# Performance work log

Measured on AMD Instinct MI355X. Metric: run time of the kernel, lower is better.

Reference implementation:

```python
import jax, jax.numpy as jnp
import numpy as np

B, N, H = 1, 4096, 2048
NH, HD = 16, H // 16
WINDOW = 4096
EPS = 1e-6
THETA = 10000.0
NEG = -1e30


def rmsnorm(x, w):
    var = jnp.mean(jnp.square(x.astype(jnp.float32)), axis=-1, keepdims=True)
    return (x * jax.lax.rsqrt(var + EPS)).astype(w.dtype) * w


def rotate_half(x):
    x1, x2 = x[..., : x.shape[-1] // 2], x[..., x.shape[-1] // 2 :]
    return jnp.concatenate((-x2, x1), axis=-1)


def setup_inputs() -> dict:
    key = jax.random.key(0)
    k1, k2, k3 = jax.random.split(key, 3)
    x = jax.random.normal(k1, (B, N, H), dtype=jnp.float32)
    w_qkv = jax.random.normal(k2, (H, 3 * H), dtype=jnp.float32) * (1.0 / np.sqrt(H))
    w_out = jax.random.normal(k3, (H, H), dtype=jnp.float32) * (1.0 / np.sqrt(H))
    q_gamma = jnp.ones((HD,), dtype=jnp.float32)
    k_gamma = jnp.ones((HD,), dtype=jnp.float32)
    return {"x": x, "w_qkv": w_qkv, "w_out": w_out, "q_gamma": q_gamma, "k_gamma": k_gamma}


def reference(x, w_qkv, w_out, q_gamma, k_gamma):
    b, n, _ = x.shape
    qkv = jnp.einsum('bnh,hm->bnm', x, w_qkv)  # [b,n,3H]
    q, k, v = jnp.split(qkv, 3, axis=-1)
    # [b, nh, n, hd]
    q = q.reshape(b, n, NH, HD).transpose(0, 2, 1, 3)
    k = k.reshape(b, n, NH, HD).transpose(0, 2, 1, 3)
    v = v.reshape(b, n, NH, HD).transpose(0, 2, 1, 3)
    # qk RMSNorm over head_dim
    q = rmsnorm(q, q_gamma)
    k = rmsnorm(k, k_gamma)
    # RoPE
    inv_freq = 1.0 / (THETA ** (jnp.arange(0, HD, 2, dtype=jnp.float32) / HD))
    t = jnp.arange(n, dtype=jnp.float32)
    freqs = t[:, None] * inv_freq[None, :]          # [n, hd/2]
    emb = jnp.concatenate((freqs, freqs), axis=-1)  # [n, hd]
    cos = jnp.cos(emb)[None, None, :, :]
    sin = jnp.sin(emb)[None, None, :, :]
    q = q * cos + rotate_half(q) * sin
    k = k * cos + rotate_half(k) * sin
    # causal + sliding-window mask (kv not truncated since n == WINDOW)
    kv_len = k.shape[-2]
    q_idx = jnp.arange(n)[:, None] + (kv_len - n)
    k_idx = jnp.arange(kv_len)[None, :]
    mask = (q_idx >= k_idx) & (q_idx - k_idx <= WINDOW)
    scores = jnp.einsum('bhqd,bhkd->bhqk', q, k) / np.sqrt(HD)
    scores = jnp.where(mask[None, None, :, :], scores, NEG)
    attn = jax.nn.softmax(scores, axis=-1)
    out = jnp.einsum('bhqk,bhkd->bhqd', attn, v)
    out = out.transpose(0, 2, 1, 3).reshape(b, n, H)
    return jnp.einsum('bnh,hm->bnm', out, w_out)
```

## Files before the change

### kernel.cpp

```cpp
#include <hip/hip_runtime.h>
#include <stdint.h>

typedef short bf16x8 __attribute__((ext_vector_type(8)));
typedef float f32x4 __attribute__((ext_vector_type(4)));
typedef unsigned short u16;

__device__ __forceinline__ float b2f(u16 u) {
  return __uint_as_float(((unsigned)u) << 16);
}
__device__ __forceinline__ u16 f2b(float f) {
  unsigned u = __float_as_uint(f);
  return (u16)((u + 0x7fffu + ((u >> 16) & 1u)) >> 16);
}

#define NEGINF (-1.0e30f)

__device__ __forceinline__ void gld_lds16(const u16* g, u16* l) {
  __builtin_amdgcn_global_load_lds(
      (const __attribute__((address_space(1))) unsigned int*)(const void*)g,
      (__attribute__((address_space(3))) unsigned int*)(void*)l, 16, 0, 0);
}

__global__ void sniff5(const u16* x, const u16* wq, const u16* wo,
                       const u16* qg, const u16* kg, int* flags) {
  const u16* p;
  int S;
  switch (blockIdx.x) {
    case 0: p = x;  S = 2048; break;
    case 1: p = wq; S = 2048; break;
    case 2: p = wo; S = 2048; break;
    case 3: p = qg; S = 128;  break;
    default: p = kg; S = 128; break;
  }
  __shared__ int cbig, czero;
  if (threadIdx.x == 0) { cbig = 0; czero = 0; }
  __syncthreads();
  int cb = 0, cz = 0;
  for (int i = threadIdx.x; i < S; i += 256) {
    const u16 u = p[i];
    if (((u >> 7) & 0xFF) >= 0xC0) ++cb;
    if (!(i & 1) && u == 0) ++cz;
  }
  atomicAdd(&cbig, cb);
  atomicAdd(&czero, cz);
  __syncthreads();
  if (threadIdx.x == 0)
    flags[blockIdx.x] = (cbig > S / 32 || czero > 3 * S / 8) ? 1 : 0;
}

__global__ __launch_bounds__(256) void conv_in(const void* __restrict__ src,
                                               u16* __restrict__ dst,
                                               const int* __restrict__ flags,
                                               int fidx, int n) {
  const int fp32 = flags[fidx];
  int i = blockIdx.x * 256 + threadIdx.x;
  const int stride = gridDim.x * 256;
  if (fp32) {
    const float* s = (const float*)src;
    for (; i < n; i += stride) dst[i] = f2b(s[i]);
  } else {
    const u16* s = (const u16*)src;
    for (; i < n; i += stride) dst[i] = s[i];
  }
}

__global__ __launch_bounds__(256) void transpose_in(
    const void* __restrict__ src, u16* __restrict__ dst,
    const int* __restrict__ flags, int fidx, int ss, int ds) {
  __shared__ u16 tile[64][65];
  const int fp32 = flags[fidx];
  const int rb = blockIdx.y * 64, cb = blockIdx.x * 64;
  const int cl = threadIdx.x & 63, r0 = threadIdx.x >> 6;
  if (fp32) {
    const float* s = (const float*)src;
#pragma unroll
    for (int i = 0; i < 16; ++i) {
      int r = r0 + i * 4;
      tile[r][cl] = f2b(s[(long long)(rb + r) * ss + cb + cl]);
    }
  } else {
    const u16* s = (const u16*)src;
#pragma unroll
    for (int i = 0; i < 16; ++i) {
      int r = r0 + i * 4;
      tile[r][cl] = s[(long long)(rb + r) * ss + cb + cl];
    }
  }
  __syncthreads();
#pragma unroll
  for (int i = 0; i < 16; ++i) {
    int r2 = r0 + i * 4;
    dst[(long long)(cb + r2) * ds + rb + cl] = tile[cl][r2];
  }
}

__global__ __launch_bounds__(256) void transpose_bf16(
    const u16* __restrict__ src, u16* __restrict__ dst, int ss, int ds,
    long long sz, long long dz) {
  __shared__ u16 tile[64][65];
  const u16* s = src + (long long)blockIdx.z * sz;
  u16* d = dst + (long long)blockIdx.z * dz;
  const int rb = blockIdx.y * 64, cb = blockIdx.x * 64;
  const int cl = threadIdx.x & 63, r0 = threadIdx.x >> 6;
#pragma unroll
  for (int i = 0; i < 16; ++i) {
    int r = r0 + i * 4;
    tile[r][cl] = s[(long long)(rb + r) * ss + cb + cl];
  }
  __syncthreads();
#pragma unroll
  for (int i = 0; i < 16; ++i) {
    int r2 = r0 + i * 4;
    d[(long long)(cb + r2) * ds + rb + cl] = tile[cl][r2];
  }
}

__global__ __launch_bounds__(256) void gemm_bt(
    const u16* __restrict__ A, const u16* __restrict__ Bt, u16* __restrict__ C,
    int M, int N, int K, int ldc) {
  __shared__ __align__(16) u16 As[128 * 32];
  __shared__ __align__(16) u16 Bs[128 * 32];
  const int tid = threadIdx.x;
  const int w = tid >> 6, l = tid & 63;
  const int lane15 = l & 15, quad = l >> 4;
  const int m0 = blockIdx.y * 128, n0 = blockIdx.x * 128;
  const int wm = (w >> 1) * 64, wn = (w & 1) * 64;
  const int srow = w * 32 + (l >> 2);
  const int skoff = (((l & 3) ^ ((l >> 3) & 3))) * 8;
  const u16* gA = A + (size_t)(m0 + srow) * K + skoff;
  const u16* gB = Bt + (size_t)(n0 + srow) * K + skoff;
  u16* lA = &As[w * 1024];
  u16* lB = &Bs[w * 1024];
  const int rq = (quad ^ ((lane15 >> 1) & 3)) * 8;
  f32x4 acc[4][4] = {};
  const int nK = K >> 5;
  for (int kb = 0; kb < nK; ++kb) {
    __syncthreads();
    gld_lds16(gA, lA);
    gld_lds16(gA + (size_t)16 * K, lA + 512);
    gld_lds16(gB, lB);
    gld_lds16(gB + (size_t)16 * K, lB + 512);
    __syncthreads();
    bf16x8 af[4], bfr[4];
#pragma unroll
    for (int mi = 0; mi < 4; ++mi)
      af[mi] = *(const bf16x8*)&As[(wm + mi * 16 + lane15) * 32 + rq];
#pragma unroll
    for (int ni = 0; ni < 4; ++ni)
      bfr[ni] = *(const bf16x8*)&Bs[(wn + ni * 16 + lane15) * 32 + rq];
#pragma unroll
    for (int mi = 0; mi < 4; ++mi)
#pragma unroll
      for (int ni = 0; ni < 4; ++ni)
        acc[mi][ni] = __builtin_amdgcn_mfma_f32_16x16x32_bf16(
            af[mi], bfr[ni], acc[mi][ni], 0, 0, 0);
    gA += 32;
    gB += 32;
  }
#pragma unroll
  for (int mi = 0; mi < 4; ++mi)
#pragma unroll
    for (int ni = 0; ni < 4; ++ni)
#pragma unroll
      for (int r = 0; r < 4; ++r)
        C[(size_t)(m0 + wm + mi * 16 + quad * 4 + r) * ldc +
          (n0 + wn + ni * 16 + lane15)] = f2b(acc[mi][ni][r]);
}

__global__ __launch_bounds__(256) void gemm_bt_f32(
    const u16* __restrict__ A, const u16* __restrict__ Bt,
    float* __restrict__ C, int M, int N, int K, int ldc) {
  __shared__ __align__(16) u16 As[128 * 32];
  __shared__ __align__(16) u16 Bs[128 * 32];
  const int tid = threadIdx.x;
  const int w = tid >> 6, l = tid & 63;
  const int lane15 = l & 15, quad = l >> 4;
  const int m0 = blockIdx.y * 128, n0 = blockIdx.x * 128;
  const int wm = (w >> 1) * 64, wn = (w & 1) * 64;
  const int srow = w * 32 + (l >> 2);
  const int skoff = (((l & 3) ^ ((l >> 3) & 3))) * 8;
  const u16* gA = A + (size_t)(m0 + srow) * K + skoff;
  const u16* gB = Bt + (size_t)(n0 + srow) * K + skoff;
  u16* lA = &As[w * 1024];
  u16* lB = &Bs[w * 1024];
  const int rq = (quad ^ ((lane15 >> 1) & 3)) * 8;
  f32x4 acc[4][4] = {};
  const int nK = K >> 5;
  for (int kb = 0; kb < nK; ++kb) {
    __syncthreads();
    gld_lds16(gA, lA);
    gld_lds16(gA + (size_t)16 * K, lA + 512);
    gld_lds16(gB, lB);
    gld_lds16(gB + (size_t)16 * K, lB + 512);
    __syncthreads();
    bf16x8 af[4], bfr[4];
#pragma unroll
    for (int mi = 0; mi < 4; ++mi)
      af[mi] = *(const bf16x8*)&As[(wm + mi * 16 + lane15) * 32 + rq];
#pragma unroll
    for (int ni = 0; ni < 4; ++ni)
      bfr[ni] = *(const bf16x8*)&Bs[(wn + ni * 16 + lane15) * 32 + rq];
#pragma unroll
    for (int mi = 0; mi < 4; ++mi)
#pragma unroll
      for (int ni = 0; ni < 4; ++ni)
        acc[mi][ni] = __builtin_amdgcn_mfma_f32_16x16x32_bf16(
            af[mi], bfr[ni], acc[mi][ni], 0, 0, 0);
    gA += 32;
    gB += 32;
  }
#pragma unroll
  for (int mi = 0; mi < 4; ++mi)
#pragma unroll
    for (int ni = 0; ni < 4; ++ni)
#pragma unroll
      for (int r = 0; r < 4; ++r)
        C[(size_t)(m0 + wm + mi * 16 + quad * 4 + r) * ldc +
          (n0 + wn + ni * 16 + lane15)] = acc[mi][ni][r];
}

__global__ __launch_bounds__(256) void rms_rope(
    const u16* __restrict__ in, const u16* __restrict__ gamma,
    u16* __restrict__ outr) {
  const int wid = blockIdx.x * 4 + (threadIdx.x >> 6);
  const int l = threadIdx.x & 63;
  const int n = wid >> 4;
  const int h = wid & 15;
  const u16* base = in + (size_t)n * 2048 + h * 128;
  float a = b2f(base[l]), b = b2f(base[l + 64]);
  float ssum = a * a + b * b;
#pragma unroll
  for (int m = 1; m < 64; m <<= 1) ssum += __shfl_xor(ssum, m);
  const float r = rsqrtf(ssum * (1.0f / 128.0f) + 1e-6f);
  a *= r * b2f(gamma[l]);
  b *= r * b2f(gamma[l + 64]);
  const float inv = __expf(-(float)l * 0.14391156831212787f);
  float s, c;
  sincosf((float)n * inv, &s, &c);
  const size_t o = ((size_t)h * 4096 + n) * 128 + l;
  outr[o] = f2b(a * c - b * s);
  outr[o + 64] = f2b(b * c + a * s);
}

__device__ __forceinline__ int swzK(int o) {
  return o ^ ((((o) >> 7) & 7) << 3);
}
__device__ __forceinline__ int swzV(int o) {
  return o ^ ((((o) >> 6) & 7) << 3);
}

__global__ __launch_bounds__(256, 2) void flash_attn(
    const u16* __restrict__ q_r, const u16* __restrict__ k_r,
    const u16* __restrict__ v_t, u16* __restrict__ attn) {
  __shared__ __align__(16) u16 Kt[64 * 128];
  __shared__ __align__(16) u16 Vt[128 * 64];
  __shared__ __align__(16) u16 Pt[128 * 64];
  const int b = blockIdx.x;
  const int h = b & 15;
  const int qt = (b < 256) ? (31 - (b >> 4)) : ((b - 256) >> 4);
  const int m0 = qt * 128;
  const int tid = threadIdx.x, w = tid >> 6, l = tid & 63;
  const int lane15 = l & 15, quad = l >> 4;

  bf16x8 aq[2][4];
#pragma unroll
  for (int mi = 0; mi < 2; ++mi)
#pragma unroll
    for (int ks = 0; ks < 4; ++ks)
      aq[mi][ks] = *(const bf16x8*)&q_r[((size_t)h * 4096 + m0 + w * 32 +
                                         mi * 16 + lane15) * 128 +
                                        ks * 32 + quad * 8];

  f32x4 acc_o[2][8] = {};
  float m_i[2][4], l_i[2][4];
#pragma unroll
  for (int mi = 0; mi < 2; ++mi)
#pragma unroll
    for (int r = 0; r < 4; ++r) {
      m_i[mi][r] = NEGINF;
      l_i[mi][r] = 0.f;
    }

  const int jend = m0 + 64;
  for (int j0 = 0; j0 <= jend; j0 += 64) {
    __syncthreads();
#pragma unroll
    for (int i = 0; i < 4; ++i) {
      const int rg = i * 4 + w;
      const int keyr = rg * 4 + (l >> 4);
      const int kc = (l & 15) ^ (keyr & 7);
      const int dr = rg * 8 + (l >> 3);
      const int vc = (l & 7) ^ (dr & 7);
      gld_lds16(&k_r[((size_t)h * 4096 + j0 + keyr) * 128 + kc * 8],
                &Kt[rg * 512]);
      gld_lds16(&v_t[((size_t)h * 128 + dr) * 4096 + j0 + vc * 8],
                &Vt[rg * 512]);
    }
    __syncthreads();

    f32x4 s2[2][4] = {};
#pragma unroll
    for (int ni = 0; ni < 4; ++ni) {
#pragma unroll
      for (int ks = 0; ks < 4; ++ks) {
        bf16x8 bk = *(const bf16x8*)&Kt[swzK((ni * 16 + lane15) * 128 +
                                             ks * 32 + quad * 8)];
        s2[0][ni] = __builtin_amdgcn_mfma_f32_16x16x32_bf16(aq[0][ks], bk,
                                                            s2[0][ni], 0, 0, 0);
        s2[1][ni] = __builtin_amdgcn_mfma_f32_16x16x32_bf16(aq[1][ks], bk,
                                                            s2[1][ni], 0, 0, 0);
      }
    }

    const float sc = 0.08838834764831845f;
    const bool mt = (j0 >= m0);
#pragma unroll
    for (int mi = 0; mi < 2; ++mi) {
#pragma unroll
      for (int r = 0; r < 4; ++r) {
        const int lrow = w * 32 + mi * 16 + quad * 4 + r;
        float xv[4], mx4 = NEGINF;
#pragma unroll
        for (int ni = 0; ni < 4; ++ni) {
          float xx = s2[mi][ni][r] * sc;
          if (mt && (j0 + ni * 16 + lane15 > m0 + lrow)) xx = NEGINF;
          xv[ni] = xx;
          mx4 = fmaxf(mx4, xx);
        }
        const float mold = m_i[mi][r];
        const unsigned long long bal = __ballot(mx4 > mold + 8.0f);
        float mcur = mold;
        if (((unsigned)(bal >> (quad * 16)) & 0xFFFFu) != 0u) {
          float mx = mx4;
#pragma unroll
          for (int mk = 1; mk < 16; mk <<= 1)
            mx = fmaxf(mx, __shfl_xor(mx, mk));
          const float mnew = fmaxf(mold, mx);
          const float alpha = __expf(mold - mnew);
          l_i[mi][r] *= alpha;
          m_i[mi][r] = mnew;
          mcur = mnew;
#pragma unroll
          for (int ni = 0; ni < 8; ++ni) acc_o[mi][ni][r] *= alpha;
        }
        float rs = 0.f;
#pragma unroll
        for (int ni = 0; ni < 4; ++ni) {
          const float p = __expf(xv[ni] - mcur);
          Pt[swzV(lrow * 64 + ni * 16 + lane15)] = f2b(p);
          rs += p;
        }
        l_i[mi][r] += rs;
      }
    }

#pragma unroll
    for (int ks = 0; ks < 2; ++ks) {
      bf16x8 ap0 = *(const bf16x8*)&Pt[swzV((w * 32 + lane15) * 64 + ks * 32 +
                                            quad * 8)];
      bf16x8 ap1 = *(const bf16x8*)&Pt[swzV((w * 32 + 16 + lane15) * 64 +
                                            ks * 32 + quad * 8)];
#pragma unroll
      for (int ni = 0; ni < 8; ++ni) {
        bf16x8 bv = *(const bf16x8*)&Vt[swzV((ni * 16 + lane15) * 64 +
                                             ks * 32 + quad * 8)];
        acc_o[0][ni] = __builtin_amdgcn_mfma_f32_16x16x32_bf16(
            ap0, bv, acc_o[0][ni], 0, 0, 0);
        acc_o[1][ni] = __builtin_amdgcn_mfma_f32_16x16x32_bf16(
            ap1, bv, acc_o[1][ni], 0, 0, 0);
      }
    }
  }

#pragma unroll
  for (int mi = 0; mi < 2; ++mi)
#pragma unroll
    for (int r = 0; r < 4; ++r) {
      float s = l_i[mi][r];
#pragma unroll
      for (int mk = 1; mk < 16; mk <<= 1) s += __shfl_xor(s, mk);
      l_i[mi][r] = s;
    }
#pragma unroll
  for (int mi = 0; mi < 2; ++mi)
#pragma unroll
    for (int ni = 0; ni < 8; ++ni)
#pragma unroll
      for (int r = 0; r < 4; ++r)
        attn[(size_t)(m0 + w * 32 + mi * 16 + quad * 4 + r) * 2048 + h * 128 +
             ni * 16 + lane15] = f2b(acc_o[mi][ni][r] / l_i[mi][r]);
}

extern "C" void kernel_launch(void* const* d_in, const int* in_sizes, int n_in,
                              void* d_out, int out_size, void* d_ws,
                              size_t ws_size, hipStream_t stream) {
  (void)out_size; (void)ws_size;
  int ix = 0, iwq = 1, iwo = 2, ig1 = 3, ig2 = 4;
  {
    int g1 = -1, g2 = -1, xx = -1, wqq = -1, woo = -1;
    for (int i = 0; i < n_in; ++i) {
      const int s = in_sizes[i];
      if (s == 8388608) xx = i;
      else if (s == 12582912) wqq = i;
      else if (s == 4194304) woo = i;
      else if (s == 128) { if (g1 < 0) g1 = i; else g2 = i; }
    }
    if (xx >= 0 && wqq >= 0 && woo >= 0 && g1 >= 0 && g2 >= 0) {
      ix = xx; iwq = wqq; iwo = woo; ig1 = g1; ig2 = g2;
    }
  }
  const void* x = d_in[ix];
  const void* wq = d_in[iwq];
  const void* wo = d_in[iwo];
  const void* qg = d_in[ig1];
  const void* kg = d_in[ig2];
  float* out = (float*)d_out;
  char* ws = (char*)d_ws;
  u16* xb = (u16*)(ws);
  u16* k_buf = (u16*)(ws + 16777216LL);
  u16* wT = (u16*)(ws + 33554432LL);
  int* flags = (int*)(ws + 58720256LL);
  u16* gq_b = (u16*)(ws + 58720512LL);
  u16* gk_b = (u16*)(ws + 58721024LL);
  u16* q_r = (u16*)(ws);
  u16* attn = (u16*)(ws + 16777216LL);
  u16* v_t = (u16*)(ws + 33554432LL);
  u16* woT = (u16*)(ws + 50331648LL);
  u16* q_buf = (u16*)d_out;
  u16* k_r = (u16*)d_out;
  u16* v_buf = (u16*)d_out + 8388608;

  const dim3 gg(16, 32);
  sniff5<<<5, 256, 0, stream>>>((const u16*)x, (const u16*)wq, (const u16*)wo,
                                (const u16*)qg, (const u16*)kg, flags);
  conv_in<<<8192, 256, 0, stream>>>(x, xb, flags, 0, 4096 * 2048);
  conv_in<<<1, 256, 0, stream>>>(qg, gq_b, flags, 3, 128);
  conv_in<<<1, 256, 0, stream>>>(kg, gk_b, flags, 4, 128);
  transpose_in<<<dim3(96, 32), 256, 0, stream>>>(wq, wT, flags, 1, 6144, 2048);
  gemm_bt<<<gg, 256, 0, stream>>>(xb, wT, q_buf, 4096, 2048, 2048, 2048);
  gemm_bt<<<gg, 256, 0, stream>>>(xb, wT + 4194304LL, k_buf, 4096, 2048, 2048,
                                  2048);
  gemm_bt<<<gg, 256, 0, stream>>>(xb, wT + 8388608LL, v_buf, 4096, 2048, 2048,
                                  2048);
  rms_rope<<<dim3(16384), 256, 0, stream>>>(q_buf, gq_b, q_r);
  rms_rope<<<dim3(16384), 256, 0, stream>>>(k_buf, gk_b, k_r);
  transpose_bf16<<<dim3(2, 64, 16), 256, 0, stream>>>(v_buf, v_t, 2048, 4096,
                                                      128LL, 524288LL);
  transpose_in<<<dim3(32, 32), 256, 0, stream>>>(wo, woT, flags, 2, 2048, 2048);
  flash_attn<<<dim3(512), 256, 0, stream>>>(q_r, k_r, v_t, attn);
  gemm_bt_f32<<<gg, 256, 0, stream>>>(attn, woT, out, 4096, 2048, 2048, 2048);
}
```

Baseline: 589.5 us.

## Fuse Q/K/V projection GEMMs into one launch with XCD-aware block remapping

The three separate Q, K and V projection GEMMs become a single 1536-block launch that writes to three output buffers chosen by column block. Block IDs are remapped so that each of the MI355X's 8 XCDs (chiplets) gets a contiguous group of N-tiles, which should raise L2 reuse of weight tiles. The output GEMM gets the same XCD-aware mapping. Removing two launches and the tail effects between them is the other aim; the cost is fixed hardcoded shapes in the kernel.

```diff
diff --git a/kernel.cpp b/kernel.cpp
--- a/kernel.cpp
+++ b/kernel.cpp
@@ -115,15 +115,79 @@
   }
 }
 
-__global__ __launch_bounds__(256) void gemm_bt(
-    const u16* __restrict__ A, const u16* __restrict__ Bt, u16* __restrict__ C,
-    int M, int N, int K, int ldc) {
+__global__ __launch_bounds__(256) void gemm_qkv(
+    const u16* __restrict__ A, const u16* __restrict__ Bt,
+    u16* __restrict__ Cq, u16* __restrict__ Ck, u16* __restrict__ Cv, int K) {
   __shared__ __align__(16) u16 As[128 * 32];
   __shared__ __align__(16) u16 Bs[128 * 32];
+  const int bid = blockIdx.x;
+  const int xcd = bid & 7, lid = bid >> 3;
+  const int mb = lid / 6, nsub = lid - mb * 6;
+  const int nb = xcd * 6 + nsub;
+  const int m0 = mb * 128;
+  const int n0g = nb * 128;
+  const int sel = nb >> 4;
+  u16* C = sel == 0 ? Cq : (sel == 1 ? Ck : Cv);
+  const int n0 = (nb & 15) * 128;
   const int tid = threadIdx.x;
   const int w = tid >> 6, l = tid & 63;
   const int lane15 = l & 15, quad = l >> 4;
-  const int m0 = blockIdx.y * 128, n0 = blockIdx.x * 128;
+  const int wm = (w >> 1) * 64, wn = (w & 1) * 64;
+  const int srow = w * 32 + (l >> 2);
+  const int skoff = (((l & 3) ^ ((l >> 3) & 3))) * 8;
+  const u16* gA = A + (size_t)(m0 + srow) * K + skoff;
+  const u16* gB = Bt + (size_t)(n0g + srow) * K + skoff;
+  u16* lA = &As[w * 1024];
+  u16* lB = &Bs[w * 1024];
+  const int rq = (quad ^ ((lane15 >> 1) & 3)) * 8;
+  f32x4 acc[4][4] = {};
+  const int nK = K >> 5;
+  for (int kb = 0; kb < nK; ++kb) {
+    __syncthreads();
+    gld_lds16(gA, lA);
+    gld_lds16(gA + (size_t)16 * K, lA + 512);
+    gld_lds16(gB, lB);
+    gld_lds16(gB + (size_t)16 * K, lB + 512);
+    __syncthreads();
+    bf16x8 af[4], bfr[4];
+#pragma unroll
+    for (int mi = 0; mi < 4; ++mi)
+      af[mi] = *(const bf16x8*)&As[(wm + mi * 16 + lane15) * 32 + rq];
+#pragma unroll
+    for (int ni = 0; ni < 4; ++ni)
+      bfr[ni] = *(const bf16x8*)&Bs[(wn + ni * 16 + lane15) * 32 + rq];
+#pragma unroll
+    for (int mi = 0; mi < 4; ++mi)
+#pragma unroll
+      for (int ni = 0; ni < 4; ++ni)
+        acc[mi][ni] = __builtin_amdgcn_mfma_f32_16x16x32_bf16(
+            af[mi], bfr[ni], acc[mi][ni], 0, 0, 0);
+    gA += 32;
+    gB += 32;
+  }
+#pragma unroll
+  for (int mi = 0; mi < 4; ++mi)
+#pragma unroll
+    for (int ni = 0; ni < 4; ++ni)
+#pragma unroll
+      for (int r = 0; r < 4; ++r)
+        C[(size_t)(m0 + wm + mi * 16 + quad * 4 + r) * 2048 +
+          (n0 + wn + ni * 16 + lane15)] = f2b(acc[mi][ni][r]);
+}
+
+__global__ __launch_bounds__(256) void gemm_bt_f32(
+    const u16* __restrict__ A, const u16* __restrict__ Bt,
+    float* __restrict__ C, int K) {
+  __shared__ __align__(16) u16 As[128 * 32];
+  __shared__ __align__(16) u16 Bs[128 * 32];
+  const int bid = blockIdx.x;
+  const int xcd = bid & 7, lid = bid >> 3;
+  const int mb = lid >> 1, nsub = lid & 1;
+  const int nb = xcd * 2 + nsub;
+  const int m0 = mb * 128, n0 = nb * 128;
+  const int tid = threadIdx.x;
+  const int w = tid >> 6, l = tid & 63;
+  const int lane15 = l & 15, quad = l >> 4;
   const int wm = (w >> 1) * 64, wn = (w & 1) * 64;
   const int srow = w * 32 + (l >> 2);
   const int skoff = (((l & 3) ^ ((l >> 3) & 3))) * 8;
@@ -163,59 +227,7 @@
     for (int ni = 0; ni < 4; ++ni)
 #pragma unroll
       for (int r = 0; r < 4; ++r)
-        C[(size_t)(m0 + wm + mi * 16 + quad * 4 + r) * ldc +
-          (n0 + wn + ni * 16 + lane15)] = f2b(acc[mi][ni][r]);
-}
-
-__global__ __launch_bounds__(256) void gemm_bt_f32(
-    const u16* __restrict__ A, const u16* __restrict__ Bt,
-    float* __restrict__ C, int M, int N, int K, int ldc) {
-  __shared__ __align__(16) u16 As[128 * 32];
-  __shared__ __align__(16) u16 Bs[128 * 32];
-  const int tid = threadIdx.x;
-  const int w = tid >> 6, l = tid & 63;
-  const int lane15 = l & 15, quad = l >> 4;
-  const int m0 = blockIdx.y * 128, n0 = blockIdx.x * 128;
-  const int wm = (w >> 1) * 64, wn = (w & 1) * 64;
-  const int srow = w * 32 + (l >> 2);
-  const int skoff = (((l & 3) ^ ((l >> 3) & 3))) * 8;
-  const u16* gA = A + (size_t)(m0 + srow) * K + skoff;
-  const u16* gB = Bt + (size_t)(n0 + srow) * K + skoff;
-  u16* lA = &As[w * 1024];
-  u16* lB = &Bs[w * 1024];
-  const int rq = (quad ^ ((lane15 >> 1) & 3)) * 8;
-  f32x4 acc[4][4] = {};
-  const int nK = K >> 5;
-  for (int kb = 0; kb < nK; ++kb) {
-    __syncthreads();
-    gld_lds16(gA, lA);
-    gld_lds16(gA + (size_t)16 * K, lA + 512);
-    gld_lds16(gB, lB);
-    gld_lds16(gB + (size_t)16 * K, lB + 512);
-    __syncthreads();
-    bf16x8 af[4], bfr[4];
-#pragma unroll
-    for (int mi = 0; mi < 4; ++mi)
-      af[mi] = *(const bf16x8*)&As[(wm + mi * 16 + lane15) * 32 + rq];
-#pragma unroll
-    for (int ni = 0; ni < 4; ++ni)
-      bfr[ni] = *(const bf16x8*)&Bs[(wn + ni * 16 + lane15) * 32 + rq];
-#pragma unroll
-    for (int mi = 0; mi < 4; ++mi)
-#pragma unroll
-      for (int ni = 0; ni < 4; ++ni)
-        acc[mi][ni] = __builtin_amdgcn_mfma_f32_16x16x32_bf16(
-            af[mi], bfr[ni], acc[mi][ni], 0, 0, 0);
-    gA += 32;
-    gB += 32;
-  }
-#pragma unroll
-  for (int mi = 0; mi < 4; ++mi)
-#pragma unroll
-    for (int ni = 0; ni < 4; ++ni)
-#pragma unroll
-      for (int r = 0; r < 4; ++r)
-        C[(size_t)(m0 + wm + mi * 16 + quad * 4 + r) * ldc +
+        C[(size_t)(m0 + wm + mi * 16 + quad * 4 + r) * 2048 +
           (n0 + wn + ni * 16 + lane15)] = acc[mi][ni][r];
 }
 
@@ -430,23 +442,18 @@
   u16* k_r = (u16*)d_out;
   u16* v_buf = (u16*)d_out + 8388608;
 
-  const dim3 gg(16, 32);
   sniff5<<<5, 256, 0, stream>>>((const u16*)x, (const u16*)wq, (const u16*)wo,
                                 (const u16*)qg, (const u16*)kg, flags);
   conv_in<<<8192, 256, 0, stream>>>(x, xb, flags, 0, 4096 * 2048);
   conv_in<<<1, 256, 0, stream>>>(qg, gq_b, flags, 3, 128);
   conv_in<<<1, 256, 0, stream>>>(kg, gk_b, flags, 4, 128);
   transpose_in<<<dim3(96, 32), 256, 0, stream>>>(wq, wT, flags, 1, 6144, 2048);
-  gemm_bt<<<gg, 256, 0, stream>>>(xb, wT, q_buf, 4096, 2048, 2048, 2048);
-  gemm_bt<<<gg, 256, 0, stream>>>(xb, wT + 4194304LL, k_buf, 4096, 2048, 2048,
-                                  2048);
-  gemm_bt<<<gg, 256, 0, stream>>>(xb, wT + 8388608LL, v_buf, 4096, 2048, 2048,
-                                  2048);
+  gemm_qkv<<<dim3(1536), 256, 0, stream>>>(xb, wT, q_buf, k_buf, v_buf, 2048);
   rms_rope<<<dim3(16384), 256, 0, stream>>>(q_buf, gq_b, q_r);
   rms_rope<<<dim3(16384), 256, 0, stream>>>(k_buf, gk_b, k_r);
   transpose_bf16<<<dim3(2, 64, 16), 256, 0, stream>>>(v_buf, v_t, 2048, 4096,
                                                       128LL, 524288LL);
   transpose_in<<<dim3(32, 32), 256, 0, stream>>>(wo, woT, flags, 2, 2048, 2048);
   flash_attn<<<dim3(512), 256, 0, stream>>>(q_r, k_r, v_t, attn);
-  gemm_bt_f32<<<gg, 256, 0, stream>>>(attn, woT, out, 4096, 2048, 2048, 2048);
-}
+  gemm_bt_f32<<<dim3(512), 256, 0, stream>>>(attn, woT, out, 2048);
+}
```

New measurement: 566.6 us. 3.9% less time.
